# Kernel optimization log

Measured on AMD Instinct MI355X. Metric: run time of the kernel, lower is better.

## Reference

```python
import jax, jax.numpy as jnp
import numpy as np
from jax import lax

BS, L, NB = 16, 50, 64          # batch, seq_length, num_blk_pervisit
D = 256                          # d_model
BLK_D = 768                      # frozen block-embedding dim
N_BLK = 65536                    # block vocab size
MEM_SIZE = 64                    # mem_size == mem_update_size (required for stackable memory)
MEM_UPDATE = 64
EPS = 1e-5


def _blk_trans(x, w1, b1, w2, b2, g, b):
    # Linear(768->2D) + ReLU + Linear(2D->D) + LayerNorm(D); dropout omitted (eval mode)
    h = jax.nn.relu(x @ w1 + b1)
    y = h @ w2 + b2
    mu = jnp.mean(y, axis=-1, keepdims=True)
    var = jnp.mean((y - mu) ** 2, axis=-1, keepdims=True)
    return g * (y - mu) * lax.rsqrt(var + EPS) + b


def setup_inputs() -> dict:
    key = jax.random.key(0)
    ks = jax.random.split(key, 16)
    s = 0.02
    f32 = jnp.float32
    return {
        "v_all": jax.random.normal(ks[0], (BS, L, D), f32),
        "transformed_v_all": jax.random.normal(ks[1], (BS, L, D), f32),
        "blk_emb_w": jax.random.normal(ks[2], (N_BLK, BLK_D), f32) * s,
        "bt_w1": jax.random.normal(ks[3], (BLK_D, 2 * D), f32) * s,
        "bt_b1": jnp.zeros((2 * D,), f32),
        "bt_w2": jax.random.normal(ks[4], (2 * D, D), f32) * s,
        "bt_b2": jnp.zeros((D,), f32),
        "bt_g": jnp.ones((D,), f32),
        "bt_b": jnp.zeros((D,), f32),
        "wq": jax.random.normal(ks[5], (D, D), f32) * s,
        "wk": jax.random.normal(ks[6], (D, D), f32) * s,
        "am_w1": jax.random.normal(ks[7], (2 * D, D), f32) * s,
        "am_b1": jnp.zeros((D,), f32),
        "am_w2": jax.random.normal(ks[8], (D, 1), f32) * s,
        "out_w": jax.random.normal(ks[9], (2 * D, 2), f32) * s,
        "out_b": jnp.zeros((2,), f32),
        "input_txt": jax.random.randint(ks[10], (BS, L, NB), 0, N_BLK, dtype=jnp.int32),
        "masks_txt": jax.random.randint(ks[11], (BS, L, NB), 0, 2, dtype=jnp.int32),
        "lengths": jax.random.randint(ks[12], (BS,), 2, L + 1, dtype=jnp.int32),
    }


def reference(v_all, transformed_v_all, blk_emb_w, bt_w1, bt_b1, bt_w2, bt_b2,
              bt_g, bt_b, wq, wk, am_w1, am_b1, am_w2, out_w, out_b,
              input_txt, masks_txt, lengths):
    bt = (bt_w1, bt_b1, bt_w2, bt_b2, bt_g, bt_b)

    # --- per-visit block selection (att_mlp + topk gather) ---
    v_text = _blk_trans(blk_emb_w[input_txt], *bt)                 # [BS,L,NB,D]
    tv = jnp.broadcast_to(transformed_v_all[:, :, None, :], v_text.shape)
    att_in = jnp.concatenate([tv, v_text], axis=-1)                # [BS,L,NB,2D]
    score = (jnp.tanh(att_in @ am_w1 + am_b1) @ am_w2)[..., 0]     # [BS,L,NB]
    score = jax.nn.softmax(score, axis=-1)
    score = jnp.where(masks_txt == 0, 0.0, score)
    idx = lax.top_k(score, MEM_UPDATE)[1]                          # [BS,L,MU]
    sel_ids = jnp.take_along_axis(input_txt, idx, axis=2)          # [BS,L,MU]
    sel_mask = jnp.take_along_axis(masks_txt, idx, axis=2)

    # --- sequential memory update recurrence ---
    query = transformed_v_all + v_all                              # [BS,L,D]
    scale = jnp.sqrt(jnp.float32(D))

    def step(carry, xs):
        ids, mk = carry                                            # [BS, M]
        nids, nmk, q = xs                                          # [BS,MU], [BS,MU], [BS,D]
        mem_in = jnp.concatenate([ids, nids], axis=1)              # [BS, 2M]
        mask_in = jnp.concatenate([mk, nmk], axis=1)
        x = _blk_trans(blk_emb_w[mem_in], *bt)                     # [BS,2M,D]
        e = jnp.einsum("bd,bmd->bm", q @ wq, x @ wk) / scale
        att = jnp.where(mask_in == 0, 0.0, jax.nn.softmax(e, axis=-1))
        tki = lax.top_k(att, MEM_SIZE)[1]                          # [BS, M]
        oi = jnp.take_along_axis(mem_in, tki, axis=1)
        om = jnp.take_along_axis(mask_in, tki, axis=1)
        return (oi, om), oi

    xs = (jnp.swapaxes(sel_ids[:, 1:], 0, 1),
          jnp.swapaxes(sel_mask[:, 1:], 0, 1),
          jnp.swapaxes(query[:, 1:], 0, 1))
    _, ys = lax.scan(step, (sel_ids[:, 0], sel_mask[:, 0]), xs)    # [L-1,BS,M]
    mem_stack = jnp.swapaxes(ys, 0, 1)                             # [BS,L-1,M] == memory[1:]
    memory_final = jnp.take_along_axis(
        mem_stack, (lengths - 2)[:, None, None], axis=1)[:, 0]      # [BS,M]

    # --- pooling + output head ---
    vmask = jnp.arange(L)[None, :] < lengths[:, None]              # length-masked max pool
    v_final = jnp.max(jnp.where(vmask[:, :, None], transformed_v_all, -jnp.inf), axis=1)
    mem_vec_final = jnp.max(_blk_trans(blk_emb_w[memory_final], *bt), axis=1)
    output = jnp.concatenate([v_final, mem_vec_final], axis=1) @ out_w + out_b
    return (output, memory_final)
```

## Files before the change

kernel.cpp:

```cpp
#include <hip/hip_runtime.h>
#include <math.h>

constexpr int kBS   = 16;
constexpr int kL    = 50;
constexpr int kNB   = 64;
constexpr int kD    = 256;
constexpr int kNBLK = 65536;
constexpr int kMaxUsed = 51200;

#define NEG_HUGE (-3.402823466e38f)

typedef _Float16 h8 __attribute__((ext_vector_type(8)));
typedef _Float16 h4 __attribute__((ext_vector_type(4)));
typedef float f32x4 __attribute__((ext_vector_type(4)));

__device__ __forceinline__ unsigned f2sort(float f) {
    unsigned u = __float_as_uint(f);
    return (u & 0x80000000u) ? ~u : (u | 0x80000000u);
}

__device__ __forceinline__ void bitonic_u64(unsigned long long* s, int i, int n) {
    for (int k = 2; k <= n; k <<= 1) {
        for (int j = k >> 1; j > 0; j >>= 1) {
            __syncthreads();
            int ixj = i ^ j;
            if (ixj > i) {
                unsigned long long x = s[i], y = s[ixj];
                bool sw = ((i & k) == 0) ? (x > y) : (x < y);
                if (sw) { s[i] = y; s[ixj] = x; }
            }
        }
    }
    __syncthreads();
}

__global__ void k_clear(int* __restrict__ flags) {
    flags[blockIdx.x * 256 + threadIdx.x] = 0;
}
__global__ void k_mark(const int* __restrict__ ids, int* __restrict__ flags, int n) {
    int i = blockIdx.x * 256 + threadIdx.x;
    if (i < n) flags[ids[i]] = 1;
}
__global__ void k_scan_a(const int* __restrict__ flags, int* __restrict__ slots,
                         int* __restrict__ bsum) {
    int i = blockIdx.x * 256 + threadIdx.x;
    __shared__ int s[256];
    int v = flags[i];
    s[threadIdx.x] = v; __syncthreads();
    for (int o = 1; o < 256; o <<= 1) {
        int t2 = (threadIdx.x >= o) ? s[threadIdx.x - o] : 0;
        __syncthreads();
        s[threadIdx.x] += t2;
        __syncthreads();
    }
    slots[i] = s[threadIdx.x] - v;
    if (threadIdx.x == 255) bsum[blockIdx.x] = s[255];
}
__global__ void k_scan_b(int* __restrict__ bsum, int* __restrict__ mcount) {
    __shared__ int s[256];
    int v = bsum[threadIdx.x];
    s[threadIdx.x] = v; __syncthreads();
    for (int o = 1; o < 256; o <<= 1) {
        int t2 = (threadIdx.x >= o) ? s[threadIdx.x - o] : 0;
        __syncthreads();
        s[threadIdx.x] += t2;
        __syncthreads();
    }
    bsum[threadIdx.x] = s[threadIdx.x] - v;
    if (threadIdx.x == 255) *mcount = s[255];
}
__global__ void k_scan_c(const int* __restrict__ flags, int* __restrict__ slots,
                         const int* __restrict__ bsum, int* __restrict__ ulist) {
    int i = blockIdx.x * 256 + threadIdx.x;
    int slot = slots[i] + bsum[blockIdx.x];
    slots[i] = slot;
    if (flags[i]) ulist[slot] = i;
}

__global__ void k_split_bT(const float* __restrict__ B, int ldb, int K,
                           _Float16* __restrict__ Ph, _Float16* __restrict__ Pl,
                           int row_off, int ldp, float scale)
{
    int n = blockIdx.x;
    for (int k = threadIdx.x; k < K; k += 256) {
        float v = B[(long long)k * ldb + n] * scale;
        _Float16 h = (_Float16)v;
        _Float16 l = (_Float16)(v - (float)h);
        Ph[(long long)(row_off + n) * ldp + k] = h;
        Pl[(long long)(row_off + n) * ldp + k] = l;
    }
}

__global__ __launch_bounds__(256) void gemm_mfma3(
    const float* __restrict__ A, int lda,
    const int* __restrict__ gather, const float* __restrict__ A2,
    const _Float16* __restrict__ Bh, const _Float16* __restrict__ Bl,
    float* __restrict__ C, int ldc,
    int Mstatic, const int* __restrict__ mcount,
    int K, const float* __restrict__ bias, int relu,
    float ascale, float inv_scale)
{
    int mlim = Mstatic;
    if (mcount) mlim = *mcount;
    const int bm = blockIdx.x * 128;
    if (bm >= mlim) return;
    const int bn = blockIdx.y * 128;

    __shared__ _Float16 Ash[128][40];
    __shared__ _Float16 Asl[128][40];
    __shared__ _Float16 Bsh[128][40];
    __shared__ _Float16 Bsl[128][40];

    const int t = threadIdx.x;

    const float* aptr[4];
    const float* aptr2[4];
    int arow[4], aoff[4];
    #pragma unroll
    for (int i = 0; i < 4; ++i) {
        int c = t + i * 256;
        int r = c >> 3, o = (c & 7) * 4;
        arow[i] = r; aoff[i] = o;
        int grow = bm + r;
        long long g = 0;
        if (grow < mlim) g = gather ? (long long)gather[grow] : (long long)grow;
        aptr[i]  = A + g * lda + o;
        aptr2[i] = A2 ? (A2 + g * lda + o) : nullptr;
    }
    const _Float16* bptr[4];
    int brow[4], boff[4], bpl[4];
    #pragma unroll
    for (int i = 0; i < 4; ++i) {
        int c = t + i * 256;
        int pl = c >> 9, cc = c & 511;
        int r = cc >> 2, o = (cc & 3) * 8;
        brow[i] = r; boff[i] = o; bpl[i] = pl;
        bptr[i] = (pl ? Bl : Bh) + (long long)(bn + r) * K + o;
    }

    f32x4 acc[4][4];
    #pragma unroll
    for (int m = 0; m < 4; ++m)
        #pragma unroll
        for (int n = 0; n < 4; ++n)
            acc[m][n] = (f32x4){0.f, 0.f, 0.f, 0.f};

    const int lane = t & 63;
    const int wid  = t >> 6;
    const int wr = (wid >> 1) * 64, wc = (wid & 1) * 64;
    const int fr = lane & 15, fk = (lane >> 4) * 8;

    float4 pa[4], pa2[4];
    h8 pb[4];
    #pragma unroll
    for (int i = 0; i < 4; ++i) {
        pa[i] = *(const float4*)(aptr[i]);
        if (A2) pa2[i] = *(const float4*)(aptr2[i]);
        pb[i] = *(const h8*)(bptr[i]);
    }

    const int nt = K / 32;
    for (int tI = 0; tI < nt; ++tI) {
        __syncthreads();
        #pragma unroll
        for (int i = 0; i < 4; ++i) {
            float vx = pa[i].x, vy = pa[i].y, vz = pa[i].z, vw = pa[i].w;
            if (A2) { vx += pa2[i].x; vy += pa2[i].y; vz += pa2[i].z; vw += pa2[i].w; }
            vx *= ascale; vy *= ascale; vz *= ascale; vw *= ascale;
            h4 hh, ll;
            hh[0] = (_Float16)vx; ll[0] = (_Float16)(vx - (float)hh[0]);
            hh[1] = (_Float16)vy; ll[1] = (_Float16)(vy - (float)hh[1]);
            hh[2] = (_Float16)vz; ll[2] = (_Float16)(vz - (float)hh[2]);
            hh[3] = (_Float16)vw; ll[3] = (_Float16)(vw - (float)hh[3]);
            *(h4*)&Ash[arow[i]][aoff[i]] = hh;
            *(h4*)&Asl[arow[i]][aoff[i]] = ll;
        }
        #pragma unroll
        for (int i = 0; i < 4; ++i) {
            _Float16* dst = bpl[i] ? &Bsl[brow[i]][boff[i]] : &Bsh[brow[i]][boff[i]];
            *(h8*)dst = pb[i];
        }
        __syncthreads();
        if (tI + 1 < nt) {
            int k0 = (tI + 1) * 32;
            #pragma unroll
            for (int i = 0; i < 4; ++i) {
                pa[i] = *(const float4*)(aptr[i] + k0);
                if (A2) pa2[i] = *(const float4*)(aptr2[i] + k0);
                pb[i] = *(const h8*)(bptr[i] + k0);
            }
        }
        h8 ah_[4], al_[4];
        #pragma unroll
        for (int m = 0; m < 4; ++m) {
            ah_[m] = *(const h8*)&Ash[wr + m * 16 + fr][fk];
            al_[m] = *(const h8*)&Asl[wr + m * 16 + fr][fk];
        }
        #pragma unroll
        for (int n = 0; n < 4; ++n) {
            h8 bh_ = *(const h8*)&Bsh[wc + n * 16 + fr][fk];
            h8 bl_ = *(const h8*)&Bsl[wc + n * 16 + fr][fk];
            #pragma unroll
            for (int m = 0; m < 4; ++m) {
                acc[m][n] = __builtin_amdgcn_mfma_f32_16x16x32_f16(ah_[m], bh_, acc[m][n], 0, 0, 0);
                acc[m][n] = __builtin_amdgcn_mfma_f32_16x16x32_f16(ah_[m], bl_, acc[m][n], 0, 0, 0);
                acc[m][n] = __builtin_amdgcn_mfma_f32_16x16x32_f16(al_[m], bh_, acc[m][n], 0, 0, 0);
            }
        }
    }

    const int cr0 = (lane >> 4) * 4;
    #pragma unroll
    for (int m = 0; m < 4; ++m) {
        #pragma unroll
        for (int r = 0; r < 4; ++r) {
            int row = bm + wr + m * 16 + cr0 + r;
            if (row >= mlim) continue;
            float* crow = C + (long long)row * ldc;
            #pragma unroll
            for (int n = 0; n < 4; ++n) {
                int col = bn + wc + n * 16 + fr;
                float v = acc[m][n][r] * inv_scale;
                if (bias) v += bias[col];
                if (relu) v = fmaxf(v, 0.f);
                crow[col] = v;
            }
        }
    }
}

__global__ __launch_bounds__(256) void ln256_inplace(
    float* __restrict__ Y, const float* __restrict__ g, const float* __restrict__ b,
    int Mstatic, const int* __restrict__ mcount)
{
    int row = blockIdx.x;
    int mlim = mcount ? *mcount : Mstatic;
    if (row >= mlim) return;
    int d = threadIdx.x;
    float v = Y[(long long)row * 256 + d];
    __shared__ float red[256];
    red[d] = v; __syncthreads();
    for (int off = 128; off; off >>= 1) { if (d < off) red[d] += red[d + off]; __syncthreads(); }
    float mu = red[0] * (1.f / 256.f);
    __syncthreads();
    float dv = v - mu;
    red[d] = dv * dv; __syncthreads();
    for (int off = 128; off; off >>= 1) { if (d < off) red[d] += red[d + off]; __syncthreads(); }
    float var = red[0] * (1.f / 256.f);
    float out = g[d] * dv * (1.f / sqrtf(var + 1e-5f)) + b[d];
    Y[(long long)row * 256 + d] = out;
}

__global__ __launch_bounds__(256) void p1score(
    const float* __restrict__ tvp, const float* __restrict__ AK,
    const int* __restrict__ slots, const float* __restrict__ am_w2,
    const int* __restrict__ ids, float* __restrict__ scores)
{
    int bl = blockIdx.x;
    int lane = threadIdx.x & 63;
    int wv   = threadIdx.x >> 6;
    float4 tv = *(const float4*)(tvp + (long long)bl * 256 + lane * 4);
    float4 w2 = *(const float4*)(am_w2 + lane * 4);
    for (int s = wv * 16; s < wv * 16 + 16; ++s) {
        int slot = slots[ids[bl * 64 + s]];
        float4 a = *(const float4*)(AK + (long long)slot * 512 + lane * 4);
        double p = (double)tanhf(tv.x + a.x) * w2.x
                 + (double)tanhf(tv.y + a.y) * w2.y
                 + (double)tanhf(tv.z + a.z) * w2.z
                 + (double)tanhf(tv.w + a.w) * w2.w;
        #pragma unroll
        for (int off = 32; off; off >>= 1) p += __shfl_down(p, off);
        if (lane == 0) scores[bl * 64 + s] = (float)p;
    }
}

__global__ __launch_bounds__(64) void p1sort(
    const float* __restrict__ scores, const int* __restrict__ ids_in,
    const int* __restrict__ mk_in, int* __restrict__ sel_ids, int* __restrict__ sel_mk)
{
    int bl = blockIdx.x;
    int i = threadIdx.x;
    __shared__ unsigned long long s[64];
    float sc = scores[bl * 64 + i];
    int mk = mk_in[bl * 64 + i];
    float key = mk ? sc : NEG_HUGE;
    s[i] = ((unsigned long long)(~f2sort(key)) << 32) | (unsigned)i;
    bitonic_u64(s, i, 64);
    int src = (int)(unsigned)(s[i] & 0xffffffffull);
    sel_ids[bl * 64 + i] = ids_in[bl * 64 + src];
    sel_mk [bl * 64 + i] = mk_in [bl * 64 + src];
}

__global__ __launch_bounds__(256) void etab2(
    const float* __restrict__ qw, const float* __restrict__ AK,
    const int* __restrict__ slots, const int* __restrict__ sel_ids,
    float* __restrict__ E)
{
    const int l = blockIdx.x;
    const int b = blockIdx.y;
    __shared__ float Ks[16][64];
    __shared__ float Qs[16][68];
    __shared__ int rowA[64];
    const int t  = threadIdx.x;
    const int tx = t & 15, ty = t >> 4;
    if (t < 64) rowA[t] = slots[sel_ids[(b * kL + l) * 64 + t]];
    __syncthreads();

    const int rA = t >> 2;
    const int kA = (t & 3) * 4;
    const float* aptr = AK + (long long)rowA[rA] * 512 + 256 + kA;
    const float* qbase = qw + ((long long)b * kL + 1) * 256;
    const bool tsok = rA < 49;

    double acc[4][4];
    #pragma unroll
    for (int i = 0; i < 4; ++i)
        #pragma unroll
        for (int j = 0; j < 4; ++j) acc[i][j] = 0.0;

    for (int k0 = 0; k0 < 256; k0 += 16) {
        float4 av = *(const float4*)(aptr + k0);
        float4 bv = make_float4(0.f, 0.f, 0.f, 0.f);
        if (tsok) bv = *(const float4*)(qbase + (long long)rA * 256 + k0 + kA);
        __syncthreads();
        Ks[kA + 0][rA] = av.x; Ks[kA + 1][rA] = av.y;
        Ks[kA + 2][rA] = av.z; Ks[kA + 3][rA] = av.w;
        Qs[kA + 0][rA] = bv.x; Qs[kA + 1][rA] = bv.y;
        Qs[kA + 2][rA] = bv.z; Qs[kA + 3][rA] = bv.w;
        __syncthreads();
        #pragma unroll
        for (int k = 0; k < 16; ++k) {
            float a[4], q[4];
            *(float4*)&a[0] = *(const float4*)&Ks[k][tx * 4];
            *(float4*)&q[0] = *(const float4*)&Qs[k][ty * 4];
            #pragma unroll
            for (int i = 0; i < 4; ++i)
                #pragma unroll
                for (int j = 0; j < 4; ++j)
                    acc[i][j] += (double)a[i] * (double)q[j];
        }
    }
    #pragma unroll
    for (int j = 0; j < 4; ++j) {
        int ts = ty * 4 + j;
        if (ts >= 49) continue;
        #pragma unroll
        for (int i = 0; i < 4; ++i) {
            int s = tx * 4 + i;
            E[((long long)b * 49 + ts) * 3200 + l * 64 + s] = (float)acc[i][j];
        }
    }
}

__global__ __launch_bounds__(64) void recur(
    const float* __restrict__ E, const int* __restrict__ sel_ids,
    const int* __restrict__ sel_mk, const int* __restrict__ lengths,
    int* __restrict__ memf, float* __restrict__ dout_mem)
{
    const int b = blockIdx.x;
    const int lane = threadIdx.x;

    int cid = sel_ids[(b * kL) * 64 + lane];
    int cmk = sel_mk [(b * kL) * 64 + lane];
    int ccd = lane;

    const int tlast = lengths[b] - 2;
    const float* Eb = E + (long long)b * 49 * 3200;

    for (int ts = 0; ts <= tlast; ++ts) {
        int nid = sel_ids[(b * kL + ts + 1) * 64 + lane];
        int nmk = sel_mk [(b * kL + ts + 1) * 64 + lane];
        const float* Et = Eb + (long long)ts * 3200;

        float k0 = cmk ? Et[ccd] : NEG_HUGE;
        float k1 = nmk ? Et[(ts + 1) * 64 + lane] : NEG_HUGE;
        unsigned long long s0 = ((unsigned long long)(~f2sort(k0)) << 32) | (unsigned)lane;
        unsigned long long s1 = ((unsigned long long)(~f2sort(k1)) << 32) | (unsigned)(64 + lane);

        #pragma unroll
        for (int k = 2; k <= 128; k <<= 1) {
            #pragma unroll
            for (int j = k >> 1; j > 0; j >>= 1) {
                if (j == 64) {
                    unsigned long long mn = s0 < s1 ? s0 : s1;
                    unsigned long long mx = s0 < s1 ? s1 : s0;
                    s0 = mn; s1 = mx;
                } else {
                    bool up   = (lane & j) == 0;
                    bool asc0 = (lane & k) == 0;
                    bool asc1 = (((lane + 64) & k) == 0);
                    unsigned long long p0 = __shfl_xor(s0, j, 64);
                    unsigned long long p1 = __shfl_xor(s1, j, 64);
                    bool km0 = (asc0 == up), km1 = (asc1 == up);
                    s0 = (km0 == (s0 < p0)) ? s0 : p0;
                    s1 = (km1 == (s1 < p1)) ? s1 : p1;
                }
            }
        }

        int src  = (int)(unsigned)(s0 & 0xffffffffull);
        int srcl = src & 63;
        int c_id = __shfl(cid, srcl, 64);
        int c_mk = __shfl(cmk, srcl, 64);
        int c_cd = __shfl(ccd, srcl, 64);
        int n_id = __shfl(nid, srcl, 64);
        int n_mk = __shfl(nmk, srcl, 64);
        bool isnew = src >= 64;
        cid = isnew ? n_id : c_id;
        cmk = isnew ? n_mk : c_mk;
        ccd = isnew ? ((ts + 1) * 64 + srcl) : c_cd;
    }

    memf[b * 64 + lane] = cid;
    dout_mem[b * 64 + lane] = (float)cid;
}

__global__ __launch_bounds__(256) void head_k(
    const float* __restrict__ tva, const int* __restrict__ lengths,
    const float* __restrict__ T, const int* __restrict__ slots,
    const int* __restrict__ memf, const float* __restrict__ out_w,
    const float* __restrict__ out_b, float* __restrict__ dout)
{
    int b = blockIdx.x, d = threadIdx.x;
    int len = lengths[b];
    float vf = NEG_HUGE;
    for (int l = 0; l < len; ++l) vf = fmaxf(vf, tva[((long long)b * kL + l) * 256 + d]);
    float mv = NEG_HUGE;
    for (int m = 0; m < 64; ++m) {
        int slot = slots[memf[b * 64 + m]];
        mv = fmaxf(mv, T[(long long)slot * 256 + d]);
    }
    double p0 = (double)vf * out_w[d * 2 + 0] + (double)mv * out_w[(256 + d) * 2 + 0];
    double p1 = (double)vf * out_w[d * 2 + 1] + (double)mv * out_w[(256 + d) * 2 + 1];
    __shared__ double r0[256], r1[256];
    r0[d] = p0; r1[d] = p1; __syncthreads();
    for (int off = 128; off; off >>= 1) {
        if (d < off) { r0[d] += r0[d + off]; r1[d] += r1[d + off]; }
        __syncthreads();
    }
    if (d == 0) {
        dout[b * 2 + 0] = (float)(r0[0] + out_b[0]);
        dout[b * 2 + 1] = (float)(r1[0] + out_b[1]);
    }
}

extern "C" void kernel_launch(void* const* d_in, const int* in_sizes, int n_in,
                              void* d_out, int out_size, void* d_ws, size_t ws_size,
                              hipStream_t stream)
{
    const float* v_all  = (const float*)d_in[0];
    const float* tva    = (const float*)d_in[1];
    const float* emb    = (const float*)d_in[2];
    const float* bt_w1  = (const float*)d_in[3];
    const float* bt_b1  = (const float*)d_in[4];
    const float* bt_w2  = (const float*)d_in[5];
    const float* bt_b2  = (const float*)d_in[6];
    const float* bt_g   = (const float*)d_in[7];
    const float* bt_bb  = (const float*)d_in[8];
    const float* wq     = (const float*)d_in[9];
    const float* wk     = (const float*)d_in[10];
    const float* am_w1  = (const float*)d_in[11];
    const float* am_b1  = (const float*)d_in[12];
    const float* am_w2  = (const float*)d_in[13];
    const float* out_w  = (const float*)d_in[14];
    const float* out_b  = (const float*)d_in[15];
    const int*   in_txt = (const int*)d_in[16];
    const int*   mk_txt = (const int*)d_in[17];
    const int*   lens   = (const int*)d_in[18];
    float* dout = (float*)d_out;

    const float S12 = 4096.f, S7 = 128.f, S8 = 256.f;
    const float INV24 = 1.f / 16777216.f;
    const float INV19 = 1.f / 524288.f;
    const float INV20 = 1.f / 1048576.f;

    size_t off = 0;
    float* W = (float*)d_ws;
    auto take = [&](size_t n) { float* p = W + off; off += (n + 3) & ~(size_t)3; return p; };
    auto takeh = [&](size_t nh) { return (_Float16*)take((nh + 1) / 2); };

    float* AKp  = take((size_t)kMaxUsed * 512);
    float* Tt   = take((size_t)kMaxUsed * 256);
    float* Hp   = take((size_t)kMaxUsed * 512);
    float* Ep   = Hp;
    float* tvpP = take((size_t)800 * 256);
    float* qwP  = take((size_t)800 * 256);
    float* scP  = take((size_t)800 * 64);
    int*   selI = (int*)take((size_t)800 * 64);
    int*   selM = (int*)take((size_t)800 * 64);
    int*   flagsP = (int*)take(kNBLK);
    int*   slotsP = (int*)take(kNBLK);
    int*   ulist  = (int*)take(kNBLK);
    int*   bsum   = (int*)take(256);
    int*   mcount = (int*)take(16);
    int*   memfP  = (int*)take(1024);
    _Float16* W1h = takeh((size_t)512 * 768);
    _Float16* W1l = takeh((size_t)512 * 768);
    _Float16* W2h = takeh((size_t)256 * 512);
    _Float16* W2l = takeh((size_t)256 * 512);
    _Float16* BCh = takeh((size_t)512 * 256);
    _Float16* BCl = takeh((size_t)512 * 256);
    _Float16* ALh = takeh((size_t)256 * 256);
    _Float16* ALl = takeh((size_t)256 * 256);
    _Float16* WQh = takeh((size_t)256 * 256);
    _Float16* WQl = takeh((size_t)256 * 256);

    k_clear<<<dim3(256), dim3(256), 0, stream>>>(flagsP);
    k_mark <<<dim3(200), dim3(256), 0, stream>>>(in_txt, flagsP, 51200);
    k_scan_a<<<dim3(256), dim3(256), 0, stream>>>(flagsP, slotsP, bsum);
    k_scan_b<<<dim3(1),   dim3(256), 0, stream>>>(bsum, mcount);
    k_scan_c<<<dim3(256), dim3(256), 0, stream>>>(flagsP, slotsP, bsum, ulist);
    k_split_bT<<<dim3(512), dim3(256), 0, stream>>>(bt_w1, 512, 768, W1h, W1l, 0, 768, S12);
    k_split_bT<<<dim3(256), dim3(256), 0, stream>>>(bt_w2, 256, 512, W2h, W2l, 0, 512, S12);
    k_split_bT<<<dim3(256), dim3(256), 0, stream>>>(am_w1 + 256 * 256, 256, 256, BCh, BCl, 0,   256, S12);
    k_split_bT<<<dim3(256), dim3(256), 0, stream>>>(wk,                256, 256, BCh, BCl, 256, 256, S12);
    k_split_bT<<<dim3(256), dim3(256), 0, stream>>>(am_w1, 256, 256, ALh, ALl, 0, 256, S12);
    k_split_bT<<<dim3(256), dim3(256), 0, stream>>>(wq,    256, 256, WQh, WQl, 0, 256, S12);

    gemm_mfma3<<<dim3(7, 2), dim3(256), 0, stream>>>(
        tva, 256, nullptr, nullptr, ALh, ALl, tvpP, 256, 800, nullptr, 256, am_b1, 0, S7, INV19);
    gemm_mfma3<<<dim3(7, 2), dim3(256), 0, stream>>>(
        tva, 256, nullptr, v_all, WQh, WQl, qwP, 256, 800, nullptr, 256, nullptr, 0, S7, INV19);

    gemm_mfma3<<<dim3(kMaxUsed / 128, 4), dim3(256), 0, stream>>>(
        emb, 768, ulist, nullptr, W1h, W1l, Hp, 512, 0, mcount, 768, bt_b1, 1, S12, INV24);
    gemm_mfma3<<<dim3(kMaxUsed / 128, 2), dim3(256), 0, stream>>>(
        Hp, 512, nullptr, nullptr, W2h, W2l, Tt, 256, 0, mcount, 512, bt_b2, 0, S12, INV24);
    ln256_inplace<<<dim3(kMaxUsed), dim3(256), 0, stream>>>(Tt, bt_g, bt_bb, 0, mcount);
    gemm_mfma3<<<dim3(kMaxUsed / 128, 4), dim3(256), 0, stream>>>(
        Tt, 256, nullptr, nullptr, BCh, BCl, AKp, 512, 0, mcount, 256, nullptr, 0, S8, INV20);

    p1score<<<dim3(800), dim3(256), 0, stream>>>(tvpP, AKp, slotsP, am_w2, in_txt, scP);
    p1sort<<<dim3(800), dim3(64), 0, stream>>>(scP, in_txt, mk_txt, selI, selM);

    etab2<<<dim3(50, 16), dim3(256), 0, stream>>>(qwP, AKp, slotsP, selI, Ep);

    recur<<<dim3(16), dim3(64), 0, stream>>>(Ep, selI, selM, lens, memfP, dout + 32);

    head_k<<<dim3(16), dim3(256), 0, stream>>>(tva, lens, Tt, slotsP, memfP,
                                               out_w, out_b, dout);
}
```

Measured before the change: 582.0 us.

## Pre-split GEMM A operands to fp16 hi/lo and widen tiles to full N

Moves the fp32-to-fp16 hi/lo splitting of the A operand out of the GEMM inner loop into separate prepass kernels (gather+split for the embedding rows, chunked in two halves to reuse scratch memory). The GEMM now uses 512-thread blocks covering the full N dimension, so each A tile is loaded once instead of once per N-block. Producer GEMMs and the layernorm write split fp16 outputs directly for the next GEMM. This cuts redundant gathers and conversions, at the cost of extra intermediate writes and reads, more kernel launches and larger shared/register use per block.

New measurement: 704.3 us. +21.0%, slower.

```diff
diff --git a/kernel.cpp b/kernel.cpp
--- a/kernel.cpp
+++ b/kernel.cpp
@@ -7,11 +7,11 @@
 constexpr int kD    = 256;
 constexpr int kNBLK = 65536;
 constexpr int kMaxUsed = 51200;
+constexpr int kChunk   = 25600;
 
 #define NEG_HUGE (-3.402823466e38f)
 
 typedef _Float16 h8 __attribute__((ext_vector_type(8)));
-typedef _Float16 h4 __attribute__((ext_vector_type(4)));
 typedef float f32x4 __attribute__((ext_vector_type(4)));
 
 __device__ __forceinline__ unsigned f2sort(float f) {
@@ -91,115 +91,122 @@
     }
 }
 
-__global__ __launch_bounds__(256) void gemm_mfma3(
-    const float* __restrict__ A, int lda,
-    const int* __restrict__ gather, const float* __restrict__ A2,
+__global__ void k_split_gatherA(const float* __restrict__ emb, const int* __restrict__ ulist,
+                                const int* __restrict__ mcount, int chunk_off,
+                                _Float16* __restrict__ Ph, _Float16* __restrict__ Pl,
+                                float scale)
+{
+    int r = blockIdx.x;
+    if (chunk_off + r >= *mcount) return;
+    long long id = ulist[chunk_off + r];
+    const float* src = emb + id * 768;
+    #pragma unroll
+    for (int j = 0; j < 3; ++j) {
+        int c = threadIdx.x + j * 256;
+        float v = src[c] * scale;
+        _Float16 h = (_Float16)v;
+        Ph[(long long)r * 768 + c] = h;
+        Pl[(long long)r * 768 + c] = (_Float16)(v - (float)h);
+    }
+}
+
+__global__ void k_split_plainA(const float* __restrict__ A, const float* __restrict__ A2,
+                               _Float16* __restrict__ Ph, _Float16* __restrict__ Pl,
+                               float scale)
+{
+    int r = blockIdx.x, c = threadIdx.x;
+    float v = A[(long long)r * 256 + c];
+    if (A2) v += A2[(long long)r * 256 + c];
+    v *= scale;
+    _Float16 h = (_Float16)v;
+    Ph[(long long)r * 256 + c] = h;
+    Pl[(long long)r * 256 + c] = (_Float16)(v - (float)h);
+}
+
+template<int NFR>
+__global__ __launch_bounds__(512) void gemm_f16p(
+    const _Float16* __restrict__ Ah, const _Float16* __restrict__ Al,
     const _Float16* __restrict__ Bh, const _Float16* __restrict__ Bl,
     float* __restrict__ C, int ldc,
-    int Mstatic, const int* __restrict__ mcount,
+    _Float16* __restrict__ Ch, _Float16* __restrict__ Cl,
+    int Mstatic, const int* __restrict__ mcount, int moff,
     int K, const float* __restrict__ bias, int relu,
-    float ascale, float inv_scale)
-{
+    float inv_scale, float out_scale)
+{
+    constexpr int N  = NFR * 64;
+    constexpr int NS = NFR / 2;
     int mlim = Mstatic;
-    if (mcount) mlim = *mcount;
+    if (mcount) mlim = *mcount - moff;
     const int bm = blockIdx.x * 128;
     if (bm >= mlim) return;
-    const int bn = blockIdx.y * 128;
 
     __shared__ _Float16 Ash[128][40];
     __shared__ _Float16 Asl[128][40];
-    __shared__ _Float16 Bsh[128][40];
-    __shared__ _Float16 Bsl[128][40];
+    __shared__ _Float16 Bsh[N][40];
+    __shared__ _Float16 Bsl[N][40];
 
     const int t = threadIdx.x;
-
-    const float* aptr[4];
-    const float* aptr2[4];
-    int arow[4], aoff[4];
-    #pragma unroll
-    for (int i = 0; i < 4; ++i) {
-        int c = t + i * 256;
-        int r = c >> 3, o = (c & 7) * 4;
-        arow[i] = r; aoff[i] = o;
-        int grow = bm + r;
-        long long g = 0;
-        if (grow < mlim) g = gather ? (long long)gather[grow] : (long long)grow;
-        aptr[i]  = A + g * lda + o;
-        aptr2[i] = A2 ? (A2 + g * lda + o) : nullptr;
-    }
-    const _Float16* bptr[4];
-    int brow[4], boff[4], bpl[4];
-    #pragma unroll
-    for (int i = 0; i < 4; ++i) {
-        int c = t + i * 256;
-        int pl = c >> 9, cc = c & 511;
-        int r = cc >> 2, o = (cc & 3) * 8;
-        brow[i] = r; boff[i] = o; bpl[i] = pl;
-        bptr[i] = (pl ? Bl : Bh) + (long long)(bn + r) * K + o;
-    }
-
-    f32x4 acc[4][4];
+    const int lane = t & 63, wid = t >> 6;
+    const int wm = wid >> 2, wn = wid & 3;
+    const int fr = lane & 15, fk = (lane >> 4) * 8;
+
+    const int rowA = t >> 2;
+    const int kOff = (t & 3) * 8;
+    const _Float16* aph = Ah + (long long)(bm + rowA) * K + kOff;
+    const _Float16* apl = Al + (long long)(bm + rowA) * K + kOff;
+    const _Float16* bph[NS];
+    const _Float16* bpl[NS];
+    #pragma unroll
+    for (int s = 0; s < NS; ++s) {
+        int r = rowA + s * 128;
+        bph[s] = Bh + (long long)r * K + kOff;
+        bpl[s] = Bl + (long long)r * K + kOff;
+    }
+
+    f32x4 acc[4][NFR];
     #pragma unroll
     for (int m = 0; m < 4; ++m)
         #pragma unroll
-        for (int n = 0; n < 4; ++n)
+        for (int n = 0; n < NFR; ++n)
             acc[m][n] = (f32x4){0.f, 0.f, 0.f, 0.f};
 
-    const int lane = t & 63;
-    const int wid  = t >> 6;
-    const int wr = (wid >> 1) * 64, wc = (wid & 1) * 64;
-    const int fr = lane & 15, fk = (lane >> 4) * 8;
-
-    float4 pa[4], pa2[4];
-    h8 pb[4];
-    #pragma unroll
-    for (int i = 0; i < 4; ++i) {
-        pa[i] = *(const float4*)(aptr[i]);
-        if (A2) pa2[i] = *(const float4*)(aptr2[i]);
-        pb[i] = *(const h8*)(bptr[i]);
-    }
+    h8 pah = *(const h8*)aph;
+    h8 pal = *(const h8*)apl;
+    h8 pbh[NS], pbl[NS];
+    #pragma unroll
+    for (int s = 0; s < NS; ++s) { pbh[s] = *(const h8*)bph[s]; pbl[s] = *(const h8*)bpl[s]; }
 
     const int nt = K / 32;
     for (int tI = 0; tI < nt; ++tI) {
         __syncthreads();
-        #pragma unroll
-        for (int i = 0; i < 4; ++i) {
-            float vx = pa[i].x, vy = pa[i].y, vz = pa[i].z, vw = pa[i].w;
-            if (A2) { vx += pa2[i].x; vy += pa2[i].y; vz += pa2[i].z; vw += pa2[i].w; }
-            vx *= ascale; vy *= ascale; vz *= ascale; vw *= ascale;
-            h4 hh, ll;
-            hh[0] = (_Float16)vx; ll[0] = (_Float16)(vx - (float)hh[0]);
-            hh[1] = (_Float16)vy; ll[1] = (_Float16)(vy - (float)hh[1]);
-            hh[2] = (_Float16)vz; ll[2] = (_Float16)(vz - (float)hh[2]);
-            hh[3] = (_Float16)vw; ll[3] = (_Float16)(vw - (float)hh[3]);
-            *(h4*)&Ash[arow[i]][aoff[i]] = hh;
-            *(h4*)&Asl[arow[i]][aoff[i]] = ll;
-        }
-        #pragma unroll
-        for (int i = 0; i < 4; ++i) {
-            _Float16* dst = bpl[i] ? &Bsl[brow[i]][boff[i]] : &Bsh[brow[i]][boff[i]];
-            *(h8*)dst = pb[i];
+        *(h8*)&Ash[rowA][kOff] = pah;
+        *(h8*)&Asl[rowA][kOff] = pal;
+        #pragma unroll
+        for (int s = 0; s < NS; ++s) {
+            *(h8*)&Bsh[rowA + s * 128][kOff] = pbh[s];
+            *(h8*)&Bsl[rowA + s * 128][kOff] = pbl[s];
         }
         __syncthreads();
         if (tI + 1 < nt) {
             int k0 = (tI + 1) * 32;
+            pah = *(const h8*)(aph + k0);
+            pal = *(const h8*)(apl + k0);
             #pragma unroll
-            for (int i = 0; i < 4; ++i) {
-                pa[i] = *(const float4*)(aptr[i] + k0);
-                if (A2) pa2[i] = *(const float4*)(aptr2[i] + k0);
-                pb[i] = *(const h8*)(bptr[i] + k0);
+            for (int s = 0; s < NS; ++s) {
+                pbh[s] = *(const h8*)(bph[s] + k0);
+                pbl[s] = *(const h8*)(bpl[s] + k0);
             }
         }
         h8 ah_[4], al_[4];
         #pragma unroll
         for (int m = 0; m < 4; ++m) {
-            ah_[m] = *(const h8*)&Ash[wr + m * 16 + fr][fk];
-            al_[m] = *(const h8*)&Asl[wr + m * 16 + fr][fk];
-        }
-        #pragma unroll
-        for (int n = 0; n < 4; ++n) {
-            h8 bh_ = *(const h8*)&Bsh[wc + n * 16 + fr][fk];
-            h8 bl_ = *(const h8*)&Bsl[wc + n * 16 + fr][fk];
+            ah_[m] = *(const h8*)&Ash[wm * 64 + m * 16 + fr][fk];
+            al_[m] = *(const h8*)&Asl[wm * 64 + m * 16 + fr][fk];
+        }
+        #pragma unroll
+        for (int n = 0; n < NFR; ++n) {
+            h8 bh_ = *(const h8*)&Bsh[wn * (NFR * 16) + n * 16 + fr][fk];
+            h8 bl_ = *(const h8*)&Bsl[wn * (NFR * 16) + n * 16 + fr][fk];
             #pragma unroll
             for (int m = 0; m < 4; ++m) {
                 acc[m][n] = __builtin_amdgcn_mfma_f32_16x16x32_f16(ah_[m], bh_, acc[m][n], 0, 0, 0);
@@ -214,24 +221,31 @@
     for (int m = 0; m < 4; ++m) {
         #pragma unroll
         for (int r = 0; r < 4; ++r) {
-            int row = bm + wr + m * 16 + cr0 + r;
+            int row = bm + wm * 64 + m * 16 + cr0 + r;
             if (row >= mlim) continue;
-            float* crow = C + (long long)row * ldc;
             #pragma unroll
-            for (int n = 0; n < 4; ++n) {
-                int col = bn + wc + n * 16 + fr;
+            for (int n = 0; n < NFR; ++n) {
+                int col = wn * (NFR * 16) + n * 16 + fr;
                 float v = acc[m][n][r] * inv_scale;
                 if (bias) v += bias[col];
                 if (relu) v = fmaxf(v, 0.f);
-                crow[col] = v;
+                if (Ch) {
+                    float w = v * out_scale;
+                    _Float16 hh = (_Float16)w;
+                    Ch[(long long)row * N + col] = hh;
+                    Cl[(long long)row * N + col] = (_Float16)(w - (float)hh);
+                } else {
+                    C[(long long)row * ldc + col] = v;
+                }
             }
         }
     }
 }
 
-__global__ __launch_bounds__(256) void ln256_inplace(
+__global__ __launch_bounds__(256) void ln256_split(
     float* __restrict__ Y, const float* __restrict__ g, const float* __restrict__ b,
-    int Mstatic, const int* __restrict__ mcount)
+    int Mstatic, const int* __restrict__ mcount,
+    _Float16* __restrict__ Ph, _Float16* __restrict__ Pl, float pscale)
 {
     int row = blockIdx.x;
     int mlim = mcount ? *mcount : Mstatic;
@@ -249,6 +263,10 @@
     float var = red[0] * (1.f / 256.f);
     float out = g[d] * dv * (1.f / sqrtf(var + 1e-5f)) + b[d];
     Y[(long long)row * 256 + d] = out;
+    float w = out * pscale;
+    _Float16 hh = (_Float16)w;
+    Ph[(long long)row * 256 + d] = hh;
+    Pl[(long long)row * 256 + d] = (_Float16)(w - (float)hh);
 }
 
 __global__ __launch_bounds__(256) void p1score(
@@ -481,8 +499,11 @@
 
     float* AKp  = take((size_t)kMaxUsed * 512);
     float* Tt   = take((size_t)kMaxUsed * 256);
-    float* Hp   = take((size_t)kMaxUsed * 512);
-    float* Ep   = Hp;
+    _Float16* Hph = takeh((size_t)kMaxUsed * 512);
+    _Float16* Hpl = takeh((size_t)kMaxUsed * 512);
+    _Float16* Tth = takeh((size_t)kMaxUsed * 256);
+    _Float16* Ttl = takeh((size_t)kMaxUsed * 256);
+    float* Ep   = take((size_t)16 * 49 * 3200);
     float* tvpP = take((size_t)800 * 256);
     float* qwP  = take((size_t)800 * 256);
     float* scP  = take((size_t)800 * 64);
@@ -504,6 +525,12 @@
     _Float16* ALl = takeh((size_t)256 * 256);
     _Float16* WQh = takeh((size_t)256 * 256);
     _Float16* WQl = takeh((size_t)256 * 256);
+    _Float16* TAh = takeh((size_t)896 * 256);
+    _Float16* TAl = takeh((size_t)896 * 256);
+    _Float16* QAh = takeh((size_t)896 * 256);
+    _Float16* QAl = takeh((size_t)896 * 256);
+    _Float16* Aeh = (_Float16*)AKp;
+    _Float16* Ael = Aeh + (size_t)kChunk * 768;
 
     k_clear<<<dim3(256), dim3(256), 0, stream>>>(flagsP);
     k_mark <<<dim3(200), dim3(256), 0, stream>>>(in_txt, flagsP, 51200);
@@ -516,19 +543,32 @@
     k_split_bT<<<dim3(256), dim3(256), 0, stream>>>(wk,                256, 256, BCh, BCl, 256, 256, S12);
     k_split_bT<<<dim3(256), dim3(256), 0, stream>>>(am_w1, 256, 256, ALh, ALl, 0, 256, S12);
     k_split_bT<<<dim3(256), dim3(256), 0, stream>>>(wq,    256, 256, WQh, WQl, 0, 256, S12);
-
-    gemm_mfma3<<<dim3(7, 2), dim3(256), 0, stream>>>(
-        tva, 256, nullptr, nullptr, ALh, ALl, tvpP, 256, 800, nullptr, 256, am_b1, 0, S7, INV19);
-    gemm_mfma3<<<dim3(7, 2), dim3(256), 0, stream>>>(
-        tva, 256, nullptr, v_all, WQh, WQl, qwP, 256, 800, nullptr, 256, nullptr, 0, S7, INV19);
-
-    gemm_mfma3<<<dim3(kMaxUsed / 128, 4), dim3(256), 0, stream>>>(
-        emb, 768, ulist, nullptr, W1h, W1l, Hp, 512, 0, mcount, 768, bt_b1, 1, S12, INV24);
-    gemm_mfma3<<<dim3(kMaxUsed / 128, 2), dim3(256), 0, stream>>>(
-        Hp, 512, nullptr, nullptr, W2h, W2l, Tt, 256, 0, mcount, 512, bt_b2, 0, S12, INV24);
-    ln256_inplace<<<dim3(kMaxUsed), dim3(256), 0, stream>>>(Tt, bt_g, bt_bb, 0, mcount);
-    gemm_mfma3<<<dim3(kMaxUsed / 128, 4), dim3(256), 0, stream>>>(
-        Tt, 256, nullptr, nullptr, BCh, BCl, AKp, 512, 0, mcount, 256, nullptr, 0, S8, INV20);
+    k_split_plainA<<<dim3(800), dim3(256), 0, stream>>>(tva, nullptr, TAh, TAl, S7);
+    k_split_plainA<<<dim3(800), dim3(256), 0, stream>>>(tva, v_all,  QAh, QAl, S7);
+
+    gemm_f16p<4><<<dim3(7), dim3(512), 0, stream>>>(
+        TAh, TAl, ALh, ALl, tvpP, 256, nullptr, nullptr,
+        800, nullptr, 0, 256, am_b1, 0, INV19, 1.f);
+    gemm_f16p<4><<<dim3(7), dim3(512), 0, stream>>>(
+        QAh, QAl, WQh, WQl, qwP, 256, nullptr, nullptr,
+        800, nullptr, 0, 256, nullptr, 0, INV19, 1.f);
+
+    for (int c = 0; c < 2; ++c) {
+        k_split_gatherA<<<dim3(kChunk), dim3(256), 0, stream>>>(
+            emb, ulist, mcount, c * kChunk, Aeh, Ael, S12);
+        gemm_f16p<8><<<dim3(kChunk / 128), dim3(512), 0, stream>>>(
+            Aeh, Ael, W1h, W1l, nullptr, 0,
+            Hph + (size_t)c * kChunk * 512, Hpl + (size_t)c * kChunk * 512,
+            0, mcount, c * kChunk, 768, bt_b1, 1, INV24, S12);
+    }
+    gemm_f16p<4><<<dim3(kMaxUsed / 128), dim3(512), 0, stream>>>(
+        Hph, Hpl, W2h, W2l, Tt, 256, nullptr, nullptr,
+        0, mcount, 0, 512, bt_b2, 0, INV24, 1.f);
+    ln256_split<<<dim3(kMaxUsed), dim3(256), 0, stream>>>(
+        Tt, bt_g, bt_bb, 0, mcount, Tth, Ttl, S8);
+    gemm_f16p<8><<<dim3(kMaxUsed / 128), dim3(512), 0, stream>>>(
+        Tth, Ttl, BCh, BCl, AKp, 512, nullptr, nullptr,
+        0, mcount, 0, 256, nullptr, 0, INV20, 1.f);
 
     p1score<<<dim3(800), dim3(256), 0, stream>>>(tvpP, AKp, slotsP, am_w2, in_txt, scP);
     p1sort<<<dim3(800), dim3(64), 0, stream>>>(scP, in_txt, mk_txt, selI, selM);
```
